# Performance work log

Measured on AMD Instinct MI355X. Metric: run time of the kernel, lower is better.

Reference implementation:

```python
import jax, jax.numpy as jnp
import numpy as np

N0, N1, N2 = 200000, 50000, 10000   # source nodes, hop-1 targets, final targets
D, C, DEG = 256, 40, 10


def _sage(x_src, x_tgt, row, col, n_tgt, Wl, Wr, b, reduce):
    # PyG SAGEConv: lin_l(aggr(messages)) + lin_r(x_target); bias on lin_l only
    msg = x_src[row]                                   # [E, D] gather
    if reduce == 'mean':
        s = jax.ops.segment_sum(msg, col, num_segments=n_tgt)
        cnt = jax.ops.segment_sum(jnp.ones((row.shape[0], 1), msg.dtype), col, num_segments=n_tgt)
        agg = s / jnp.maximum(cnt, 1.0)
    else:
        agg = jax.ops.segment_max(msg, col, num_segments=n_tgt)
    return agg @ Wl + b + x_tgt @ Wr


def setup_inputs() -> dict:
    key = jax.random.key(0)
    ks = jax.random.split(key, 16)
    x = jax.random.normal(ks[0], (N0, D), jnp.float32)
    # every target gets exactly DEG sampled neighbors (NeighborSampler-style)
    row0 = jax.random.randint(ks[1], (N1 * DEG,), 0, N0, jnp.int32)
    col0 = jnp.repeat(jnp.arange(N1, dtype=jnp.int32), DEG)
    edge_index0 = jnp.stack([row0, col0])
    row1 = jax.random.randint(ks[2], (N2 * DEG,), 0, N1, jnp.int32)
    col1 = jnp.repeat(jnp.arange(N2, dtype=jnp.int32), DEG)
    edge_index1 = jnp.stack([row1, col1])
    s = 1.0 / np.sqrt(D)
    w = lambda k, shp: jax.random.uniform(k, shp, jnp.float32, -s, s)
    return {
        'x': x, 'edge_index0': edge_index0, 'edge_index1': edge_index1,
        'Wl_m0': w(ks[3], (D, D)), 'Wr_m0': w(ks[4], (D, D)), 'b_m0': jnp.zeros((D,), jnp.float32),
        'Wl_x0': w(ks[5], (D, D)), 'Wr_x0': w(ks[6], (D, D)), 'b_x0': jnp.zeros((D,), jnp.float32),
        'Wl_m1': w(ks[7], (D, D)), 'Wr_m1': w(ks[8], (D, D)), 'b_m1': jnp.zeros((D,), jnp.float32),
        'Wl_x1': w(ks[9], (D, D)), 'Wr_x1': w(ks[10], (D, D)), 'b_x1': jnp.zeros((D,), jnp.float32),
        'W_post': w(ks[11], (2 * D, C)), 'b_post': jnp.zeros((C,), jnp.float32),
    }


def reference(x, edge_index0, edge_index1,
              Wl_m0, Wr_m0, b_m0, Wl_x0, Wr_x0, b_x0,
              Wl_m1, Wr_m1, b_m1, Wl_x1, Wr_x1, b_x1,
              W_post, b_post):
    row0, col0 = edge_index0[0], edge_index0[1]
    row1, col1 = edge_index1[0], edge_index1[1]
    tgt0 = x[:N1]
    h_m = jax.nn.relu(_sage(x, tgt0, row0, col0, N1, Wl_m0, Wr_m0, b_m0, 'mean'))
    h_x = jax.nn.relu(_sage(x, tgt0, row0, col0, N1, Wl_x0, Wr_x0, b_x0, 'max'))
    # NOTE: faithful to source bug: layer-1 target features are the RAW x[:size[1]]
    tgt1 = x[:N2]
    o_m = _sage(h_m, tgt1, row1, col1, N2, Wl_m1, Wr_m1, b_m1, 'mean')
    o_x = _sage(h_x, tgt1, row1, col1, N2, Wl_x1, Wr_x1, b_x1, 'max')
    out = jnp.concatenate([o_m, o_x], axis=-1) @ W_post + b_post
    return jax.nn.log_softmax(out, axis=-1)
```

## Files before the change

kernel.cpp:

```cpp
#include <hip/hip_runtime.h>
#include <hip/hip_bf16.h>
#include <math.h>

#define N0v 200000
#define N1v 50000
#define N2v 10000
#define Dv  256
#define Cv  40
#define DEGv 10

typedef __attribute__((ext_vector_type(8))) short          s16x8;
typedef __attribute__((ext_vector_type(8))) unsigned short u16x8;
typedef __attribute__((ext_vector_type(4))) float          f32x4;

static __device__ __forceinline__ unsigned short f2bf(float f) {
    __hip_bfloat16 h = __float2bfloat16(f);
    return *reinterpret_cast<unsigned short*>(&h);
}
static __device__ __forceinline__ float bf2f(unsigned short u) {
    __hip_bfloat16 h = *reinterpret_cast<__hip_bfloat16*>(&u);
    return __bfloat162float(h);
}

static __device__ __forceinline__ void gload16(const void* g, void* l) {
    __builtin_amdgcn_global_load_lds(
        (const __attribute__((address_space(1))) unsigned int*)g,
        (__attribute__((address_space(3))) unsigned int*)l, 16, 0, 0);
}

__global__ __launch_bounds__(256) void conv_wt_all_kernel(
    const float* __restrict__ Wl0, const float* __restrict__ Wr0,
    const float* __restrict__ Wl1, const float* __restrict__ Wr1,
    const float* __restrict__ Wl2, const float* __restrict__ Wr2,
    const float* __restrict__ Wl3, const float* __restrict__ Wr3,
    unsigned short* __restrict__ WT0, unsigned short* __restrict__ WT1,
    unsigned short* __restrict__ WT2, unsigned short* __restrict__ WT3)
{
    const int p = blockIdx.y;
    const float* Wl = (p == 0) ? Wl0 : (p == 1) ? Wl1 : (p == 2) ? Wl2 : Wl3;
    const float* Wr = (p == 0) ? Wr0 : (p == 1) ? Wr1 : (p == 2) ? Wr2 : Wr3;
    unsigned short* WT = (p == 0) ? WT0 : (p == 1) ? WT1 : (p == 2) ? WT2 : WT3;
    const int n = blockIdx.x;
    const int k = threadIdx.x;
    WT[(size_t)n * 512 + k]       = f2bf(Wl[(size_t)k * Dv + n]);
    WT[(size_t)n * 512 + 256 + k] = f2bf(Wr[(size_t)k * Dv + n]);
}

__global__ __launch_bounds__(256) void conv_rows_kernel(
    const float* __restrict__ src, unsigned short* __restrict__ dst, int n_elems)
{
    const int i = (blockIdx.x * 256 + threadIdx.x) * 8;
    if (i + 7 < n_elems) {
        float4 v0 = *(const float4*)(src + i);
        float4 v1 = *(const float4*)(src + i + 4);
        unsigned short o[8] = { f2bf(v0.x), f2bf(v0.y), f2bf(v0.z), f2bf(v0.w),
                                f2bf(v1.x), f2bf(v1.y), f2bf(v1.z), f2bf(v1.w) };
        *(u16x8*)(dst + i) = *(u16x8*)o;
    }
}

__global__ __launch_bounds__(256) void agg0_kernel(
    const float* __restrict__ x, const int* __restrict__ row,
    unsigned short* __restrict__ om, unsigned short* __restrict__ ox)
{
    const int t = blockIdx.x * 4 + (threadIdx.x >> 6);
    const int c = threadIdx.x & 63;
    const int eb = t * DEGv;
    float4 s = make_float4(0.f, 0.f, 0.f, 0.f);
    float4 mx = make_float4(-INFINITY, -INFINITY, -INFINITY, -INFINITY);
#pragma unroll
    for (int k = 0; k < DEGv; ++k) {
        const int r = row[eb + k];
        float4 v = ((const float4*)x)[(size_t)r * 64 + c];
        s.x += v.x; s.y += v.y; s.z += v.z; s.w += v.w;
        mx.x = fmaxf(mx.x, v.x); mx.y = fmaxf(mx.y, v.y);
        mx.z = fmaxf(mx.z, v.z); mx.w = fmaxf(mx.w, v.w);
    }
    const float inv = 1.0f / DEGv;
    unsigned short osum[4] = { f2bf(s.x * inv), f2bf(s.y * inv), f2bf(s.z * inv), f2bf(s.w * inv) };
    unsigned short omax[4] = { f2bf(mx.x), f2bf(mx.y), f2bf(mx.z), f2bf(mx.w) };
    *(uint2*)&om[(size_t)t * Dv + c * 4] = *(uint2*)osum;
    *(uint2*)&ox[(size_t)t * Dv + c * 4] = *(uint2*)omax;
}

__global__ __launch_bounds__(256) void agg1_kernel(
    const unsigned short* __restrict__ hm, const unsigned short* __restrict__ hx,
    const int* __restrict__ row,
    unsigned short* __restrict__ om, unsigned short* __restrict__ ox)
{
    const int t = blockIdx.x * 8 + (threadIdx.x >> 5);
    const int c = threadIdx.x & 31;
    const int eb = t * DEGv;
    float s[8] = {};
    float mx[8] = { -INFINITY, -INFINITY, -INFINITY, -INFINITY,
                    -INFINITY, -INFINITY, -INFINITY, -INFINITY };
#pragma unroll
    for (int k = 0; k < DEGv; ++k) {
        const int r = row[eb + k];
        u16x8 vm = ((const u16x8*)hm)[(size_t)r * 32 + c];
        u16x8 vx = ((const u16x8*)hx)[(size_t)r * 32 + c];
#pragma unroll
        for (int j = 0; j < 8; ++j) {
            s[j]  += bf2f(vm[j]);
            mx[j]  = fmaxf(mx[j], bf2f(vx[j]));
        }
    }
    const float inv = 1.0f / DEGv;
    unsigned short osum[8], omax[8];
#pragma unroll
    for (int j = 0; j < 8; ++j) { osum[j] = f2bf(s[j] * inv); omax[j] = f2bf(mx[j]); }
    *(u16x8*)&om[(size_t)t * Dv + c * 8] = *(u16x8*)osum;
    *(u16x8*)&ox[(size_t)t * Dv + c * 8] = *(u16x8*)omax;
}

template<int RELU, int OUTBF>
__global__ __launch_bounds__(256) void gemm_mfma_kernel(
    const unsigned short* __restrict__ A1a, const unsigned short* __restrict__ A1b,
    const unsigned short* __restrict__ A2,
    const unsigned short* __restrict__ WTa, const unsigned short* __restrict__ WTb,
    const float* __restrict__ biasa, const float* __restrict__ biasb,
    void* outa, void* outb, int M, int ldc, int col_step)
{
    __shared__ unsigned short Asb[128 * 32];
    __shared__ unsigned short Bsb[128 * 32];

    const int z = blockIdx.z;
    const unsigned short* A1 = z ? A1b : A1a;
    const unsigned short* WT = z ? WTb : WTa;
    const float* bias = z ? biasb : biasa;
    void* outp = z ? outb : outa;
    const int col_off = z * col_step;

    const int tid  = threadIdx.x;
    const int lane = tid & 63;
    const int w    = tid >> 6;
    const int wr   = w >> 1, wc = w & 1;
    const int m0   = blockIdx.x * 128, n0 = blockIdx.y * 128;

    const int srow = w * 32 + (lane >> 2);
    const int ca   = (lane & 3) * 8;
    int gmA0 = m0 + srow;      if (gmA0 >= M) gmA0 = M - 1;
    int gmA1 = m0 + srow + 16; if (gmA1 >= M) gmA1 = M - 1;
    const unsigned short* pA1_0 = A1 + (size_t)gmA0 * Dv + ca;
    const unsigned short* pA1_1 = A1 + (size_t)gmA1 * Dv + ca;
    const unsigned short* pA2_0 = A2 + (size_t)gmA0 * Dv + ca;
    const unsigned short* pA2_1 = A2 + (size_t)gmA1 * Dv + ca;
    const unsigned short* pB_0  = WT + (size_t)(n0 + srow) * 512 + ca;
    const unsigned short* pB_1  = WT + (size_t)(n0 + srow + 16) * 512 + ca;

    unsigned short* lA0 = &Asb[w * 1024];
    unsigned short* lA1 = &Asb[w * 1024 + 512];
    unsigned short* lB0 = &Bsb[w * 1024];
    unsigned short* lB1 = &Bsb[w * 1024 + 512];

    const int kq = (lane >> 4) * 8;
    const int fr = lane & 15;

    f32x4 acc[4][4] = {};

    for (int k0 = 0; k0 < 512; k0 += 32) {
        const unsigned short* a0 = (k0 < 256) ? pA1_0 + k0 : pA2_0 + (k0 - 256);
        const unsigned short* a1 = (k0 < 256) ? pA1_1 + k0 : pA2_1 + (k0 - 256);
        __syncthreads();
        gload16(a0, lA0);
        gload16(a1, lA1);
        gload16(pB_0 + k0, lB0);
        gload16(pB_1 + k0, lB1);
        __syncthreads();

        s16x8 af[4], bfr[4];
#pragma unroll
        for (int i = 0; i < 4; ++i) {
            af[i]  = *(const s16x8*)&Asb[(wr * 64 + i * 16 + fr) * 32 + kq];
            bfr[i] = *(const s16x8*)&Bsb[(wc * 64 + i * 16 + fr) * 32 + kq];
        }
#pragma unroll
        for (int i = 0; i < 4; ++i)
#pragma unroll
            for (int j = 0; j < 4; ++j)
                acc[i][j] = __builtin_amdgcn_mfma_f32_16x16x32_bf16(af[i], bfr[j], acc[i][j], 0, 0, 0);
    }

#pragma unroll
    for (int i = 0; i < 4; ++i) {
#pragma unroll
        for (int reg = 0; reg < 4; ++reg) {
            const int gr = m0 + wr * 64 + i * 16 + (lane >> 4) * 4 + reg;
            if (gr < M) {
#pragma unroll
                for (int j = 0; j < 4; ++j) {
                    const int gc = n0 + wc * 64 + j * 16 + fr;
                    float v = acc[i][j][reg] + bias[gc];
                    if (RELU) v = fmaxf(v, 0.0f);
                    if (OUTBF)
                        ((unsigned short*)outp)[(size_t)gr * ldc + col_off + gc] = f2bf(v);
                    else
                        ((float*)outp)[(size_t)gr * ldc + col_off + gc] = v;
                }
            }
        }
    }
}

__global__ __launch_bounds__(64) void post_kernel(
    const float* __restrict__ ocat, const float* __restrict__ Wp,
    const float* __restrict__ bp, float* __restrict__ out)
{
    __shared__ float srow[2 * Dv];
    __shared__ float slog[Cv];
    __shared__ float s_lse;

    const int t = blockIdx.x;
    const int tid = threadIdx.x;

    for (int i = tid; i < 2 * Dv; i += 64)
        srow[i] = ocat[(size_t)t * (2 * Dv) + i];
    __syncthreads();

    if (tid < Cv) {
        float acc = bp[tid];
#pragma unroll 8
        for (int k = 0; k < 2 * Dv; ++k)
            acc += srow[k] * Wp[(size_t)k * Cv + tid];
        slog[tid] = acc;
    }
    __syncthreads();

    if (tid == 0) {
        float m = slog[0];
        for (int c = 1; c < Cv; ++c) m = fmaxf(m, slog[c]);
        float s = 0.0f;
        for (int c = 0; c < Cv; ++c) s += expf(slog[c] - m);
        s_lse = m + logf(s);
    }
    __syncthreads();

    if (tid < Cv)
        out[(size_t)t * Cv + tid] = slog[tid] - s_lse;
}

extern "C" void kernel_launch(void* const* d_in, const int* in_sizes, int n_in,
                              void* d_out, int out_size, void* d_ws, size_t ws_size,
                              hipStream_t stream)
{
    const float* x      = (const float*)d_in[0];
    const int*   ei0    = (const int*)d_in[1];
    const int*   ei1    = (const int*)d_in[2];
    const float* Wl_m0  = (const float*)d_in[3];
    const float* Wr_m0  = (const float*)d_in[4];
    const float* b_m0   = (const float*)d_in[5];
    const float* Wl_x0  = (const float*)d_in[6];
    const float* Wr_x0  = (const float*)d_in[7];
    const float* b_x0   = (const float*)d_in[8];
    const float* Wl_m1  = (const float*)d_in[9];
    const float* Wr_m1  = (const float*)d_in[10];
    const float* b_m1   = (const float*)d_in[11];
    const float* Wl_x1  = (const float*)d_in[12];
    const float* Wr_x1  = (const float*)d_in[13];
    const float* b_x1   = (const float*)d_in[14];
    const float* W_post = (const float*)d_in[15];
    const float* b_post = (const float*)d_in[16];
    float* out = (float*)d_out;

    const int* row0 = ei0;
    const int* row1 = ei1;

    char* ws = (char*)d_ws;
    const size_t NB = (size_t)N1v * Dv * 2;
    unsigned short* xtb = (unsigned short*)(ws);
    unsigned short* am  = (unsigned short*)(ws + NB);
    unsigned short* ax  = (unsigned short*)(ws + 2 * NB);
    unsigned short* hm  = (unsigned short*)(ws + 3 * NB);
    unsigned short* hx  = (unsigned short*)(ws + 4 * NB);
    unsigned short* a1m = (unsigned short*)(ws + 5 * NB);
    unsigned short* a1x = a1m + (size_t)N2v * Dv;
    float*          ocat = (float*)(ws + 5 * NB + (size_t)2 * N2v * Dv * 2);
    unsigned short* WT0m = (unsigned short*)((char*)ocat + (size_t)N2v * 2 * Dv * 4);
    unsigned short* WT0x = WT0m + (size_t)256 * 512;
    unsigned short* WT1m = WT0x + (size_t)256 * 512;
    unsigned short* WT1x = WT1m + (size_t)256 * 512;

    const dim3 blk(256);

    conv_wt_all_kernel<<<dim3(256, 4), blk, 0, stream>>>(
        Wl_m0, Wr_m0, Wl_x0, Wr_x0, Wl_m1, Wr_m1, Wl_x1, Wr_x1,
        WT0m, WT0x, WT1m, WT1x);
    conv_rows_kernel<<<(N1v * Dv / 8 + 255) / 256, blk, 0, stream>>>(x, xtb, N1v * Dv);
    agg0_kernel<<<N1v / 4, blk, 0, stream>>>(x, row0, am, ax);

    gemm_mfma_kernel<1, 1><<<dim3((N1v + 127) / 128, 2, 2), blk, 0, stream>>>(
        am, ax, xtb, WT0m, WT0x, b_m0, b_x0, hm, hx, N1v, Dv, 0);

    agg1_kernel<<<N2v / 8, blk, 0, stream>>>(hm, hx, row1, a1m, a1x);
    gemm_mfma_kernel<0, 0><<<dim3((N2v + 127) / 128, 2, 2), blk, 0, stream>>>(
        a1m, a1x, xtb, WT1m, WT1x, b_m1, b_x1, ocat, ocat, N2v, 2 * Dv, Dv);

    post_kernel<<<N2v, dim3(64), 0, stream>>>(ocat, W_post, b_post, out);
}
```

Measured before the change: 249.9 us.

## Merge prep kernels, widen GEMM K-tile with XOR-swizzled LDS, store ocat as bf16

Folds the x-to-bf16 conversion and the weight transpose into one prep launch, removing one kernel launch. The MFMA GEMM now stages K-tiles of 64 instead of 32, with XOR-swizzled LDS columns to avoid bank conflicts, which halves the number of sync rounds per tile. The layer-1 GEMM output (ocat) is written as bf16 instead of fp32, cutting write and read traffic for the post kernel at the cost of extra rounding before the final linear layer and log-softmax.

New measurement: 232.7 us. 1.07x faster.

```diff
diff --git a/kernel.cpp b/kernel.cpp
--- a/kernel.cpp
+++ b/kernel.cpp
@@ -28,7 +28,8 @@
         (__attribute__((address_space(3))) unsigned int*)l, 16, 0, 0);
 }
 
-__global__ __launch_bounds__(256) void conv_wt_all_kernel(
+__global__ __launch_bounds__(256) void prep_kernel(
+    const float* __restrict__ x, unsigned short* __restrict__ xtb,
     const float* __restrict__ Wl0, const float* __restrict__ Wr0,
     const float* __restrict__ Wl1, const float* __restrict__ Wr1,
     const float* __restrict__ Wl2, const float* __restrict__ Wr2,
@@ -36,26 +37,24 @@
     unsigned short* __restrict__ WT0, unsigned short* __restrict__ WT1,
     unsigned short* __restrict__ WT2, unsigned short* __restrict__ WT3)
 {
-    const int p = blockIdx.y;
-    const float* Wl = (p == 0) ? Wl0 : (p == 1) ? Wl1 : (p == 2) ? Wl2 : Wl3;
-    const float* Wr = (p == 0) ? Wr0 : (p == 1) ? Wr1 : (p == 2) ? Wr2 : Wr3;
-    unsigned short* WT = (p == 0) ? WT0 : (p == 1) ? WT1 : (p == 2) ? WT2 : WT3;
-    const int n = blockIdx.x;
-    const int k = threadIdx.x;
-    WT[(size_t)n * 512 + k]       = f2bf(Wl[(size_t)k * Dv + n]);
-    WT[(size_t)n * 512 + 256 + k] = f2bf(Wr[(size_t)k * Dv + n]);
-}
-
-__global__ __launch_bounds__(256) void conv_rows_kernel(
-    const float* __restrict__ src, unsigned short* __restrict__ dst, int n_elems)
-{
-    const int i = (blockIdx.x * 256 + threadIdx.x) * 8;
-    if (i + 7 < n_elems) {
-        float4 v0 = *(const float4*)(src + i);
-        float4 v1 = *(const float4*)(src + i + 4);
+    const int b = blockIdx.x;
+    const int tid = threadIdx.x;
+    if (b < 6250) {
+        const int i = (b * 256 + tid) * 8;
+        float4 v0 = *(const float4*)(x + i);
+        float4 v1 = *(const float4*)(x + i + 4);
         unsigned short o[8] = { f2bf(v0.x), f2bf(v0.y), f2bf(v0.z), f2bf(v0.w),
                                 f2bf(v1.x), f2bf(v1.y), f2bf(v1.z), f2bf(v1.w) };
-        *(u16x8*)(dst + i) = *(u16x8*)o;
+        *(u16x8*)(xtb + i) = *(u16x8*)o;
+    } else {
+        const int idx = b - 6250;
+        const int p = idx >> 8;
+        const int n = idx & 255;
+        const float* Wl = (p == 0) ? Wl0 : (p == 1) ? Wl1 : (p == 2) ? Wl2 : Wl3;
+        const float* Wr = (p == 0) ? Wr0 : (p == 1) ? Wr1 : (p == 2) ? Wr2 : Wr3;
+        unsigned short* WT = (p == 0) ? WT0 : (p == 1) ? WT1 : (p == 2) ? WT2 : WT3;
+        WT[(size_t)n * 512 + tid]       = f2bf(Wl[(size_t)tid * Dv + n]);
+        WT[(size_t)n * 512 + 256 + tid] = f2bf(Wr[(size_t)tid * Dv + n]);
     }
 }
 
@@ -121,8 +120,8 @@
     const float* __restrict__ biasa, const float* __restrict__ biasb,
     void* outa, void* outb, int M, int ldc, int col_step)
 {
-    __shared__ unsigned short Asb[128 * 32];
-    __shared__ unsigned short Bsb[128 * 32];
+    __shared__ unsigned short Asb[128 * 64];
+    __shared__ unsigned short Bsb[128 * 64];
 
     const int z = blockIdx.z;
     const unsigned short* A1 = z ? A1b : A1a;
@@ -137,48 +136,60 @@
     const int wr   = w >> 1, wc = w & 1;
     const int m0   = blockIdx.x * 128, n0 = blockIdx.y * 128;
 
-    const int srow = w * 32 + (lane >> 2);
-    const int ca   = (lane & 3) * 8;
-    int gmA0 = m0 + srow;      if (gmA0 >= M) gmA0 = M - 1;
-    int gmA1 = m0 + srow + 16; if (gmA1 >= M) gmA1 = M - 1;
-    const unsigned short* pA1_0 = A1 + (size_t)gmA0 * Dv + ca;
-    const unsigned short* pA1_1 = A1 + (size_t)gmA1 * Dv + ca;
-    const unsigned short* pA2_0 = A2 + (size_t)gmA0 * Dv + ca;
-    const unsigned short* pA2_1 = A2 + (size_t)gmA1 * Dv + ca;
-    const unsigned short* pB_0  = WT + (size_t)(n0 + srow) * 512 + ca;
-    const unsigned short* pB_1  = WT + (size_t)(n0 + srow + 16) * 512 + ca;
-
-    unsigned short* lA0 = &Asb[w * 1024];
-    unsigned short* lA1 = &Asb[w * 1024 + 512];
-    unsigned short* lB0 = &Bsb[w * 1024];
-    unsigned short* lB1 = &Bsb[w * 1024 + 512];
-
-    const int kq = (lane >> 4) * 8;
+    const int lrow = lane >> 3;
+    const int scol = ((lane & 7) ^ lrow) * 8;
+
+    const unsigned short* pA1[4];
+    const unsigned short* pA2[4];
+    const unsigned short* pB[4];
+    unsigned short* lA[4];
+    unsigned short* lB[4];
+#pragma unroll
+    for (int c = 0; c < 4; ++c) {
+        const int r = w * 32 + c * 8 + lrow;
+        int gm = m0 + r; if (gm >= M) gm = M - 1;
+        pA1[c] = A1 + (size_t)gm * Dv + scol;
+        pA2[c] = A2 + (size_t)gm * Dv + scol;
+        pB[c]  = WT + (size_t)(n0 + r) * 512 + scol;
+        lA[c] = &Asb[(w * 32 + c * 8) * 64];
+        lB[c] = &Bsb[(w * 32 + c * 8) * 64];
+    }
+
     const int fr = lane & 15;
+    const int f7 = lane & 7;
 
     f32x4 acc[4][4] = {};
 
-    for (int k0 = 0; k0 < 512; k0 += 32) {
-        const unsigned short* a0 = (k0 < 256) ? pA1_0 + k0 : pA2_0 + (k0 - 256);
-        const unsigned short* a1 = (k0 < 256) ? pA1_1 + k0 : pA2_1 + (k0 - 256);
+    for (int k0 = 0; k0 < 512; k0 += 64) {
         __syncthreads();
-        gload16(a0, lA0);
-        gload16(a1, lA1);
-        gload16(pB_0 + k0, lB0);
-        gload16(pB_1 + k0, lB1);
+        if (k0 < 256) {
+#pragma unroll
+            for (int c = 0; c < 4; ++c) gload16(pA1[c] + k0, lA[c]);
+        } else {
+#pragma unroll
+            for (int c = 0; c < 4; ++c) gload16(pA2[c] + (k0 - 256), lA[c]);
+        }
+#pragma unroll
+        for (int c = 0; c < 4; ++c) gload16(pB[c] + k0, lB[c]);
         __syncthreads();
 
-        s16x8 af[4], bfr[4];
-#pragma unroll
-        for (int i = 0; i < 4; ++i) {
-            af[i]  = *(const s16x8*)&Asb[(wr * 64 + i * 16 + fr) * 32 + kq];
-            bfr[i] = *(const s16x8*)&Bsb[(wc * 64 + i * 16 + fr) * 32 + kq];
+#pragma unroll
+        for (int kk = 0; kk < 2; ++kk) {
+            const int sl = kk * 4 + (lane >> 4);
+            s16x8 af[4], bfr[4];
+#pragma unroll
+            for (int i = 0; i < 4; ++i) {
+                const int ar = wr * 64 + i * 16 + fr;
+                af[i]  = *(const s16x8*)&Asb[ar * 64 + ((sl ^ f7) << 3)];
+                const int br = wc * 64 + i * 16 + fr;
+                bfr[i] = *(const s16x8*)&Bsb[br * 64 + ((sl ^ f7) << 3)];
+            }
+#pragma unroll
+            for (int i = 0; i < 4; ++i)
+#pragma unroll
+                for (int j = 0; j < 4; ++j)
+                    acc[i][j] = __builtin_amdgcn_mfma_f32_16x16x32_bf16(af[i], bfr[j], acc[i][j], 0, 0, 0);
         }
-#pragma unroll
-        for (int i = 0; i < 4; ++i)
-#pragma unroll
-            for (int j = 0; j < 4; ++j)
-                acc[i][j] = __builtin_amdgcn_mfma_f32_16x16x32_bf16(af[i], bfr[j], acc[i][j], 0, 0, 0);
     }
 
 #pragma unroll
@@ -203,7 +214,7 @@
 }
 
 __global__ __launch_bounds__(64) void post_kernel(
-    const float* __restrict__ ocat, const float* __restrict__ Wp,
+    const unsigned short* __restrict__ ocat, const float* __restrict__ Wp,
     const float* __restrict__ bp, float* __restrict__ out)
 {
     __shared__ float srow[2 * Dv];
@@ -214,7 +225,7 @@
     const int tid = threadIdx.x;
 
     for (int i = tid; i < 2 * Dv; i += 64)
-        srow[i] = ocat[(size_t)t * (2 * Dv) + i];
+        srow[i] = bf2f(ocat[(size_t)t * (2 * Dv) + i]);
     __syncthreads();
 
     if (tid < Cv) {
@@ -274,25 +285,25 @@
     unsigned short* hx  = (unsigned short*)(ws + 4 * NB);
     unsigned short* a1m = (unsigned short*)(ws + 5 * NB);
     unsigned short* a1x = a1m + (size_t)N2v * Dv;
-    float*          ocat = (float*)(ws + 5 * NB + (size_t)2 * N2v * Dv * 2);
-    unsigned short* WT0m = (unsigned short*)((char*)ocat + (size_t)N2v * 2 * Dv * 4);
+    unsigned short* ocat = (unsigned short*)(ws + 5 * NB + (size_t)2 * N2v * Dv * 2);
+    unsigned short* WT0m = ocat + (size_t)N2v * 2 * Dv;
     unsigned short* WT0x = WT0m + (size_t)256 * 512;
     unsigned short* WT1m = WT0x + (size_t)256 * 512;
     unsigned short* WT1x = WT1m + (size_t)256 * 512;
 
     const dim3 blk(256);
 
-    conv_wt_all_kernel<<<dim3(256, 4), blk, 0, stream>>>(
+    prep_kernel<<<6250 + 1024, blk, 0, stream>>>(
+        x, xtb,
         Wl_m0, Wr_m0, Wl_x0, Wr_x0, Wl_m1, Wr_m1, Wl_x1, Wr_x1,
         WT0m, WT0x, WT1m, WT1x);
-    conv_rows_kernel<<<(N1v * Dv / 8 + 255) / 256, blk, 0, stream>>>(x, xtb, N1v * Dv);
     agg0_kernel<<<N1v / 4, blk, 0, stream>>>(x, row0, am, ax);
 
     gemm_mfma_kernel<1, 1><<<dim3((N1v + 127) / 128, 2, 2), blk, 0, stream>>>(
         am, ax, xtb, WT0m, WT0x, b_m0, b_x0, hm, hx, N1v, Dv, 0);
 
     agg1_kernel<<<N2v / 8, blk, 0, stream>>>(hm, hx, row1, a1m, a1x);
-    gemm_mfma_kernel<0, 0><<<dim3((N2v + 127) / 128, 2, 2), blk, 0, stream>>>(
+    gemm_mfma_kernel<0, 1><<<dim3((N2v + 127) / 128, 2, 2), blk, 0, stream>>>(
         a1m, a1x, xtb, WT1m, WT1x, b_m1, b_x1, ocat, ocat, N2v, 2 * Dv, Dv);
 
     post_kernel<<<N2v, dim3(64), 0, stream>>>(ocat, W_post, b_post, out);
```
